# Optimization experiments

Hardware: AMD Instinct MI355X
Metric: run time of the kernel (lower is better)

Reference implementation:

```python
import jax, jax.numpy as jnp
import numpy as np

N = 20000; E = 320000; F_IN = 128; H = 4; D = 32; HD = 128; G = 8; C = 10


def _ln(x, g, b):
    mu = x.mean(-1, keepdims=True)
    v = ((x - mu) ** 2).mean(-1, keepdims=True)
    return (x - mu) / jnp.sqrt(v + 1e-5) * g + b


def _tconv(x, src, dst, attr, Wq, Wk, Wv, We, Ws, bq, bk, bv, be, bs):
    # PyG TransformerConv (concat=True, beta=False, root_weight=True), eval mode
    n = x.shape[0]
    q = (x @ Wq + bq).reshape(n, H, D)[dst]            # [E,H,D] gather at targets i
    k = (x @ Wk + bk).reshape(n, H, D)[src]            # [E,H,D] gather at sources j
    v = (x @ Wv + bv).reshape(n, H, D)[src]
    ef = (attr @ We + be).reshape(-1, H, D)            # edge features lifted to [E,H,D]
    k = k + ef
    v = v + ef
    logit = (q * k).sum(-1) / jnp.sqrt(jnp.float32(D))  # [E,H]
    m = jax.ops.segment_max(logit, dst, num_segments=n)
    m = jnp.where(jnp.isfinite(m), m, 0.0)
    ex = jnp.exp(logit - m[dst])
    s = jax.ops.segment_sum(ex, dst, num_segments=n)
    alpha = ex / (s[dst] + 1e-16)                      # segment softmax over incoming edges
    out = jax.ops.segment_sum(v * alpha[..., None], dst, num_segments=n).reshape(n, HD)
    out = out + x @ Ws + bs                            # skip / root weight
    return out, alpha


def setup_inputs() -> dict:
    key = jax.random.key(0)
    ks = jax.random.split(key, 50)
    inp = {}
    inp["x"] = jax.random.normal(ks[0], (N, F_IN), jnp.float32)
    inp["edge_index"] = jax.random.randint(ks[1], (2, E), 0, N)
    inp["attr"] = jax.random.normal(ks[2], (E, 1), jnp.float32)
    inp["batch"] = jnp.sort(jax.random.randint(ks[3], (N,), 0, G))
    i = 4
    for l, din in zip((1, 2, 3), (F_IN, HD, HD)):
        for nm, shp in (("Wq", (din, HD)), ("Wk", (din, HD)), ("Wv", (din, HD)), ("We", (1, HD)), ("Ws", (din, HD))):
            inp[f"{nm}{l}"] = jax.random.normal(ks[i], shp, jnp.float32) * 0.05
            i += 1
        for nm in ("bq", "bk", "bv", "be", "bs"):
            inp[f"{nm}{l}"] = jnp.zeros((HD,), jnp.float32)
    inp["ln1_g"] = jnp.ones((HD,), jnp.float32); inp["ln1_b"] = jnp.zeros((HD,), jnp.float32)
    inp["ln2_g"] = jnp.ones((HD,), jnp.float32); inp["ln2_b"] = jnp.zeros((HD,), jnp.float32)
    inp["fc1_w"] = jax.random.normal(ks[i], (HD, HD), jnp.float32) * 0.05; i += 1
    inp["fc1_b"] = jnp.zeros((HD,), jnp.float32)
    inp["cln_g"] = jnp.ones((HD,), jnp.float32); inp["cln_b"] = jnp.zeros((HD,), jnp.float32)
    inp["fc2_w"] = jax.random.normal(ks[i], (HD, C), jnp.float32) * 0.05
    inp["fc2_b"] = jnp.zeros((C,), jnp.float32)
    return inp


def reference(x, edge_index, attr, batch,
              Wq1, Wk1, Wv1, We1, Ws1, bq1, bk1, bv1, be1, bs1,
              Wq2, Wk2, Wv2, We2, Ws2, bq2, bk2, bv2, be2, bs2,
              Wq3, Wk3, Wv3, We3, Ws3, bq3, bk3, bv3, be3, bs3,
              ln1_g, ln1_b, ln2_g, ln2_b,
              fc1_w, fc1_b, cln_g, cln_b, fc2_w, fc2_b):
    src, dst = edge_index[0], edge_index[1]
    h, a1 = _tconv(x, src, dst, attr, Wq1, Wk1, Wv1, We1, Ws1, bq1, bk1, bv1, be1, bs1)
    h = jax.nn.relu(_ln(h, ln1_g, ln1_b))              # dropout is identity in eval
    h, a2 = _tconv(h, src, dst, attr, Wq2, Wk2, Wv2, We2, Ws2, bq2, bk2, bv2, be2, bs2)
    h = jax.nn.relu(_ln(h, ln2_g, ln2_b))
    z, a3 = _tconv(h, src, dst, attr, Wq3, Wk3, Wv3, We3, Ws3, bq3, bk3, bv3, be3, bs3)
    # global mean pool over graphs
    cnt = jax.ops.segment_sum(jnp.ones((N,), z.dtype), batch, num_segments=G)
    z_pool = jax.ops.segment_sum(z, batch, num_segments=G) / jnp.maximum(cnt, 1.0)[:, None]
    # classifier
    hcl = jax.nn.relu(_ln(z_pool @ fc1_w + fc1_b, cln_g, cln_b))
    probs = jax.nn.softmax(hcl @ fc2_w + fc2_b, axis=1)
    z_sel = z_pool[batch[0]]
    return (z, z_sel, probs, a1, a2, a3)
```

## Files before the change

kernel.cpp:

```cpp
#include <hip/hip_runtime.h>


typedef short short8v __attribute__((ext_vector_type(8)));
typedef float f32x4 __attribute__((ext_vector_type(4)));

__device__ __forceinline__ unsigned pack_bf16_rne(float a, float b) {
    unsigned ua = __float_as_uint(a);
    ua += 0x7fffu + ((ua >> 16) & 1u);
    unsigned ub = __float_as_uint(b);
    ub += 0x7fffu + ((ub >> 16) & 1u);
    return (ua >> 16) | (ub & 0xffff0000u);
}

__device__ __forceinline__ unsigned short bf16_rne1(float a) {
    unsigned u = __float_as_uint(a);
    u += 0x7fffu + ((u >> 16) & 1u);
    return (unsigned short)(u >> 16);
}

__device__ __forceinline__ float blo(unsigned u) { return __uint_as_float(u << 16); }
__device__ __forceinline__ float bhi(unsigned u) { return __uint_as_float(u & 0xffff0000u); }

__global__ __launch_bounds__(256) void hist_kernel(const int* __restrict__ dst,
                                                   int* __restrict__ cnt, int E) {
    int e = blockIdx.x * 256 + threadIdx.x;
    if (e < E) atomicAdd(&cnt[dst[e]], 1);
}

__global__ __launch_bounds__(256) void blk_reduce_kernel(const int* __restrict__ cnt,
                                                         int* __restrict__ bsum, int n) {
    __shared__ int ws[4];
    const int i = blockIdx.x * 256 + threadIdx.x;
    const int lane = threadIdx.x & 63, wid = threadIdx.x >> 6;
    int v = (i < n) ? cnt[i] : 0;
#pragma unroll
    for (int off = 1; off < 64; off <<= 1) v += __shfl_xor(v, off);
    if (lane == 0) ws[wid] = v;
    __syncthreads();
    if (threadIdx.x == 0) bsum[blockIdx.x] = ws[0] + ws[1] + ws[2] + ws[3];
}

__global__ __launch_bounds__(1024) void blk_scan_kernel(int* __restrict__ bsum, int nb) {
    __shared__ int wls[16];
    const int tid = threadIdx.x, lane = tid & 63, wid = tid >> 6;
    int v = (tid < nb) ? bsum[tid] : 0;
    int sc = v;
#pragma unroll
    for (int off = 1; off < 64; off <<= 1) {
        int t = __shfl_up(sc, off);
        if (lane >= off) sc += t;
    }
    if (lane == 63) wls[wid] = sc;
    __syncthreads();
    if (tid == 0) {
        int run = 0;
        for (int w = 0; w < 16; ++w) { int t = wls[w]; wls[w] = run; run += t; }
    }
    __syncthreads();
    if (tid < nb) bsum[tid] = wls[wid] + sc - v;
}

__global__ __launch_bounds__(256) void rowptr_fill_kernel(const int* __restrict__ cnt,
                                                          const int* __restrict__ boff,
                                                          int* __restrict__ rowptr, int n) {
    __shared__ int wls[4];
    const int i = blockIdx.x * 256 + threadIdx.x;
    const int lane = threadIdx.x & 63, wid = threadIdx.x >> 6;
    int v = (i < n) ? cnt[i] : 0;
    int sc = v;
#pragma unroll
    for (int off = 1; off < 64; off <<= 1) {
        int t = __shfl_up(sc, off);
        if (lane >= off) sc += t;
    }
    if (lane == 63) wls[wid] = sc;
    __syncthreads();
    int add = boff[blockIdx.x];
    for (int w = 0; w < wid; ++w) add += wls[w];
    if (i < n) rowptr[i + 1] = sc + add;
    if (i == 0) rowptr[0] = 0;
}

__global__ __launch_bounds__(256) void fill_kernel(const int* __restrict__ src,
                                                   const int* __restrict__ dst,
                                                   const float* __restrict__ attr,
                                                   const int* __restrict__ rowptr,
                                                   int* __restrict__ tmp,
                                                   int* __restrict__ src_perm,
                                                   float* __restrict__ attr_perm,
                                                   int* __restrict__ eidp, int E) {
    int e = blockIdx.x * 256 + threadIdx.x;
    if (e < E) {
        int d = dst[e];
        int p = atomicAdd(&tmp[d], 1);
        int pos = rowptr[d] + p;
        src_perm[pos] = src[e];
        attr_perm[pos] = attr[e];
        eidp[pos] = e;
    }
}

__global__ __launch_bounds__(256) void cvt_bf16_kernel(const float* __restrict__ in,
                                                       unsigned* __restrict__ outp, int n32) {
    int i = blockIdx.x * 256 + threadIdx.x;
    if (i < n32) {
        float2 v = *(const float2*)&in[(size_t)i * 2];
        outp[i] = pack_bf16_rne(v.x, v.y);
    }
}

struct W12 { const float* p[12]; };
__global__ __launch_bounds__(256) void prepack_all_kernel(W12 ws, unsigned* __restrict__ wt) {
    const int m = blockIdx.y;
    const float* W = ws.p[m];
    int idx = blockIdx.x * 256 + threadIdx.x;
    int c = idx >> 6;
    int kp = idx & 63;
    wt[(size_t)m * 8192 + (size_t)c * 64 + kp] =
        pack_bf16_rne(W[(size_t)(2 * kp) * 128 + c], W[(size_t)(2 * kp + 1) * 128 + c]);
}

__global__ __launch_bounds__(256) void gemm_mfma_kernel(
    const unsigned short* __restrict__ Xb, const unsigned short* __restrict__ wt,
    const float* __restrict__ bq, const float* __restrict__ bk,
    const float* __restrict__ bv, const float* __restrict__ bs,
    float* __restrict__ qo, unsigned short* __restrict__ ko,
    unsigned short* __restrict__ vo, float* __restrict__ so, int nrows) {
    const int lane = threadIdx.x & 63;
    const int w = threadIdx.x >> 6;
    const int m = blockIdx.y;
    const int strip = blockIdx.x * 64 + w * 16;
    const int arow = strip + (lane & 15);
    const int arow_c = min(arow, nrows - 1);
    const int kblk = (lane >> 4) * 8;
    const unsigned short* Wm = wt + (size_t)m * 16384;
    const float* bias = (m == 0) ? bq : (m == 1) ? bk : (m == 2) ? bv : bs;

    f32x4 acc[8];
#pragma unroll
    for (int f = 0; f < 8; ++f) acc[f] = (f32x4){0.f, 0.f, 0.f, 0.f};

#pragma unroll
    for (int ks = 0; ks < 4; ++ks) {
        const int k0 = ks * 32 + kblk;
        const short8v a = *(const short8v*)&Xb[(size_t)arow_c * 128 + k0];
#pragma unroll
        for (int f = 0; f < 8; ++f) {
            const short8v b = *(const short8v*)&Wm[(size_t)(f * 16 + (lane & 15)) * 128 + k0];
            acc[f] = __builtin_amdgcn_mfma_f32_16x16x32_bf16(a, b, acc[f], 0, 0, 0);
        }
    }

    const int r0 = strip + (lane >> 4) * 4;
#pragma unroll
    for (int f = 0; f < 8; ++f) {
        const int col = f * 16 + (lane & 15);
        const float bv_ = bias[col];
        if (m == 0 || m == 3) {
            float* OUT = (m == 0) ? qo : so;
#pragma unroll
            for (int r = 0; r < 4; ++r) {
                int row = r0 + r;
                if (row < nrows) OUT[(size_t)row * 128 + col] = acc[f][r] + bv_;
            }
        } else {
            unsigned short* OUT = (m == 1) ? ko : vo;
#pragma unroll
            for (int r = 0; r < 4; ++r) {
                int row = r0 + r;
                if (row < nrows) OUT[(size_t)row * 128 + col] = bf16_rne1(acc[f][r] + bv_);
            }
        }
    }
}

__global__ __launch_bounds__(256) void node_fused_kernel(
    const float* __restrict__ qb, const unsigned* __restrict__ kb,
    const unsigned* __restrict__ vb,
    const float* __restrict__ Wev, const float* __restrict__ bev,
    const int* __restrict__ rowptr, const int* __restrict__ src_perm,
    const float* __restrict__ attr_perm, const int* __restrict__ eidp,
    float* __restrict__ alpha_perm, float* __restrict__ alpha_out,
    const float* __restrict__ skip, float* __restrict__ zout,
    unsigned* __restrict__ hbout,
    const float* __restrict__ lng, const float* __restrict__ lnb,
    int do_ln, int n) {
    __shared__ float alds[4][64][4];
    const int wid = threadIdx.x >> 6;
    const int node = blockIdx.x * 4 + wid;
    const int lane = threadIdx.x & 63;
    if (node >= n) return;
    const int start = rowptr[node], end = rowptr[node + 1];
    const int deg = end - start;
    const int h = lane >> 4;
    const float we0 = Wev[2 * lane], we1 = Wev[2 * lane + 1];
    const float be0 = bev[2 * lane], be1 = bev[2 * lane + 1];
    const float2 qv = *(const float2*)&qb[(size_t)node * 128 + 2 * lane];
    const float scale = 0.17677669529663687f;
    const bool fastp = (deg <= 64);

    float acc0 = 0.f, acc1 = 0.f, sa = 0.f;

    if (deg > 0 && fastp) {
        float pw = qv.x * we0 + qv.y * we1;
        float pb = qv.x * be0 + qv.y * be1;
#pragma unroll
        for (int off = 1; off < 16; off <<= 1) {
            pw += __shfl_xor(pw, off);
            pb += __shfl_xor(pb, off);
        }

        const bool valid = lane < deg;
        const int j = start + lane;
        const int sj = valid ? src_perm[j] : 0;
        const float aj = valid ? attr_perm[j] : 0.f;

        int t = 0;
        for (; t + 3 < deg; t += 4) {
            const int s0 = __shfl(sj, t), s1 = __shfl(sj, t + 1);
            const int s2 = __shfl(sj, t + 2), s3 = __shfl(sj, t + 3);
            const float a0 = __shfl(aj, t), a1 = __shfl(aj, t + 1);
            const float a2 = __shfl(aj, t + 2), a3 = __shfl(aj, t + 3);
            const unsigned u0 = kb[(size_t)s0 * 64 + lane];
            const unsigned u1 = kb[(size_t)s1 * 64 + lane];
            const unsigned u2 = kb[(size_t)s2 * 64 + lane];
            const unsigned u3 = kb[(size_t)s3 * 64 + lane];
            float p0 = qv.x * blo(u0) + qv.y * bhi(u0);
            float p1 = qv.x * blo(u1) + qv.y * bhi(u1);
            float p2 = qv.x * blo(u2) + qv.y * bhi(u2);
            float p3 = qv.x * blo(u3) + qv.y * bhi(u3);
#pragma unroll
            for (int off = 1; off < 16; off <<= 1) {
                p0 += __shfl_xor(p0, off); p1 += __shfl_xor(p1, off);
                p2 += __shfl_xor(p2, off); p3 += __shfl_xor(p3, off);
            }
            if ((lane & 15) == 0) {
                alds[wid][t + 0][h] = (p0 + a0 * pw + pb) * scale;
                alds[wid][t + 1][h] = (p1 + a1 * pw + pb) * scale;
                alds[wid][t + 2][h] = (p2 + a2 * pw + pb) * scale;
                alds[wid][t + 3][h] = (p3 + a3 * pw + pb) * scale;
            }
        }
        for (; t < deg; ++t) {
            const int s0 = __shfl(sj, t);
            const float a0 = __shfl(aj, t);
            const unsigned u0 = kb[(size_t)s0 * 64 + lane];
            float p0 = qv.x * blo(u0) + qv.y * bhi(u0);
#pragma unroll
            for (int off = 1; off < 16; off <<= 1) p0 += __shfl_xor(p0, off);
            if ((lane & 15) == 0) alds[wid][t][h] = (p0 + a0 * pw + pb) * scale;
        }

        float4 lg = valid ? *(const float4*)&alds[wid][lane][0]
                          : make_float4(-1e30f, -1e30f, -1e30f, -1e30f);
        float4 mx = lg;
#pragma unroll
        for (int off = 1; off < 64; off <<= 1) {
            mx.x = fmaxf(mx.x, __shfl_xor(mx.x, off));
            mx.y = fmaxf(mx.y, __shfl_xor(mx.y, off));
            mx.z = fmaxf(mx.z, __shfl_xor(mx.z, off));
            mx.w = fmaxf(mx.w, __shfl_xor(mx.w, off));
        }
        float4 ev;
        ev.x = __expf(lg.x - mx.x); ev.y = __expf(lg.y - mx.y);
        ev.z = __expf(lg.z - mx.z); ev.w = __expf(lg.w - mx.w);
        float4 s4 = ev;
#pragma unroll
        for (int off = 1; off < 64; off <<= 1) {
            s4.x += __shfl_xor(s4.x, off); s4.y += __shfl_xor(s4.y, off);
            s4.z += __shfl_xor(s4.z, off); s4.w += __shfl_xor(s4.w, off);
        }
        float4 al;
        al.x = ev.x / (s4.x + 1e-16f); al.y = ev.y / (s4.y + 1e-16f);
        al.z = ev.z / (s4.z + 1e-16f); al.w = ev.w / (s4.w + 1e-16f);
        if (valid) *(float4*)&alpha_out[(size_t)eidp[j] * 4] = al;
        *(float4*)&alds[wid][lane][0] = al;

        t = 0;
        for (; t + 3 < deg; t += 4) {
            const int s0 = __shfl(sj, t), s1 = __shfl(sj, t + 1);
            const int s2 = __shfl(sj, t + 2), s3 = __shfl(sj, t + 3);
            const float a0 = __shfl(aj, t), a1 = __shfl(aj, t + 1);
            const float a2 = __shfl(aj, t + 2), a3 = __shfl(aj, t + 3);
            const float w0 = alds[wid][t + 0][h];
            const float w1 = alds[wid][t + 1][h];
            const float w2 = alds[wid][t + 2][h];
            const float w3 = alds[wid][t + 3][h];
            const unsigned u0 = vb[(size_t)s0 * 64 + lane];
            const unsigned u1 = vb[(size_t)s1 * 64 + lane];
            const unsigned u2 = vb[(size_t)s2 * 64 + lane];
            const unsigned u3 = vb[(size_t)s3 * 64 + lane];
            acc0 += w0 * blo(u0) + w1 * blo(u1) + w2 * blo(u2) + w3 * blo(u3);
            acc1 += w0 * bhi(u0) + w1 * bhi(u1) + w2 * bhi(u2) + w3 * bhi(u3);
            sa += w0 * a0 + w1 * a1 + w2 * a2 + w3 * a3;
        }
        for (; t < deg; ++t) {
            const int s0 = __shfl(sj, t);
            const float a0 = __shfl(aj, t);
            const float w0 = alds[wid][t][h];
            const unsigned u0 = vb[(size_t)s0 * 64 + lane];
            acc0 += w0 * blo(u0);
            acc1 += w0 * bhi(u0);
            sa += w0 * a0;
        }
    } else if (deg > 0) {
        float mh = -1e30f;
        for (int c0 = start; c0 < end; c0 += 64) {
            const int nc = min(64, end - c0);
            const int sj = (lane < nc) ? src_perm[c0 + lane] : 0;
            const float aj = (lane < nc) ? attr_perm[c0 + lane] : 0.f;
            int t = 0;
            for (; t + 1 < nc; t += 2) {
                const int s0 = __shfl(sj, t), s1 = __shfl(sj, t + 1);
                const float a0 = __shfl(aj, t), a1 = __shfl(aj, t + 1);
                const unsigned u0 = kb[(size_t)s0 * 64 + lane];
                const unsigned u1 = kb[(size_t)s1 * 64 + lane];
                float p0 = qv.x * (blo(u0) + a0 * we0 + be0) + qv.y * (bhi(u0) + a0 * we1 + be1);
                float p1 = qv.x * (blo(u1) + a1 * we0 + be0) + qv.y * (bhi(u1) + a1 * we1 + be1);
#pragma unroll
                for (int off = 1; off < 16; off <<= 1) {
                    p0 += __shfl_xor(p0, off);
                    p1 += __shfl_xor(p1, off);
                }
                p0 *= scale; p1 *= scale;
                mh = fmaxf(mh, fmaxf(p0, p1));
                if ((lane & 15) == 0) {
                    alpha_perm[(size_t)(c0 + t) * 4 + h] = p0;
                    alpha_perm[(size_t)(c0 + t + 1) * 4 + h] = p1;
                }
            }
            if (t < nc) {
                const int s0 = __shfl(sj, t);
                const float a0 = __shfl(aj, t);
                const unsigned u0 = kb[(size_t)s0 * 64 + lane];
                float p0 = qv.x * (blo(u0) + a0 * we0 + be0) + qv.y * (bhi(u0) + a0 * we1 + be1);
#pragma unroll
                for (int off = 1; off < 16; off <<= 1) p0 += __shfl_xor(p0, off);
                p0 *= scale;
                mh = fmaxf(mh, p0);
                if ((lane & 15) == 0) alpha_perm[(size_t)(c0 + t) * 4 + h] = p0;
            }
        }
        const float m0 = __shfl(mh, 0), m1 = __shfl(mh, 16);
        const float m2 = __shfl(mh, 32), m3 = __shfl(mh, 48);

        float4 s4 = make_float4(0.f, 0.f, 0.f, 0.f);
        for (int c0 = start; c0 < end; c0 += 64) {
            const int j = c0 + lane;
            if (j < end) {
                float4 lg = *(const float4*)&alpha_perm[(size_t)j * 4];
                lg.x = __expf(lg.x - m0); lg.y = __expf(lg.y - m1);
                lg.z = __expf(lg.z - m2); lg.w = __expf(lg.w - m3);
                *(float4*)&alpha_perm[(size_t)j * 4] = lg;
                s4.x += lg.x; s4.y += lg.y; s4.z += lg.z; s4.w += lg.w;
            }
        }
#pragma unroll
        for (int off = 1; off < 64; off <<= 1) {
            s4.x += __shfl_xor(s4.x, off); s4.y += __shfl_xor(s4.y, off);
            s4.z += __shfl_xor(s4.z, off); s4.w += __shfl_xor(s4.w, off);
        }
        const float i0 = 1.f / (s4.x + 1e-16f), i1 = 1.f / (s4.y + 1e-16f);
        const float i2 = 1.f / (s4.z + 1e-16f), i3 = 1.f / (s4.w + 1e-16f);

        for (int c0 = start; c0 < end; c0 += 64) {
            const int nc = min(64, end - c0);
            const int j = c0 + lane;
            if (lane < nc) {
                float4 ex = *(const float4*)&alpha_perm[(size_t)j * 4];
                float4 al;
                al.x = ex.x * i0; al.y = ex.y * i1; al.z = ex.z * i2; al.w = ex.w * i3;
                *(float4*)&alpha_out[(size_t)eidp[j] * 4] = al;
                *(float4*)&alds[wid][lane][0] = al;
            }
            const int sj = (lane < nc) ? src_perm[j] : 0;
            const float aj = (lane < nc) ? attr_perm[j] : 0.f;
            int t = 0;
            for (; t + 1 < nc; t += 2) {
                const int s0 = __shfl(sj, t), s1 = __shfl(sj, t + 1);
                const float a0 = __shfl(aj, t), a1 = __shfl(aj, t + 1);
                const float w0 = alds[wid][t][h];
                const float w1 = alds[wid][t + 1][h];
                const unsigned u0 = vb[(size_t)s0 * 64 + lane];
                const unsigned u1 = vb[(size_t)s1 * 64 + lane];
                acc0 += w0 * (blo(u0) + a0 * we0 + be0) + w1 * (blo(u1) + a1 * we0 + be0);
                acc1 += w0 * (bhi(u0) + a0 * we1 + be1) + w1 * (bhi(u1) + a1 * we1 + be1);
            }
            if (t < nc) {
                const int s0 = __shfl(sj, t);
                const float a0 = __shfl(aj, t);
                const float w0 = alds[wid][t][h];
                const unsigned u0 = vb[(size_t)s0 * 64 + lane];
                acc0 += w0 * (blo(u0) + a0 * we0 + be0);
                acc1 += w0 * (bhi(u0) + a0 * we1 + be1);
            }
        }
    }

    float2 o = *(const float2*)&skip[(size_t)node * 128 + 2 * lane];
    if (deg > 0) {
        if (fastp) {
            o.x += acc0 + sa * we0 + be0;
            o.y += acc1 + sa * we1 + be1;
        } else {
            o.x += acc0;
            o.y += acc1;
        }
    }
    if (do_ln) {
        float s = o.x + o.y;
#pragma unroll
        for (int off = 1; off < 64; off <<= 1) s += __shfl_xor(s, off);
        const float mu = s * (1.f / 128.f);
        const float d0 = o.x - mu, d1 = o.y - mu;
        float vs = d0 * d0 + d1 * d1;
#pragma unroll
        for (int off = 1; off < 64; off <<= 1) vs += __shfl_xor(vs, off);
        const float inv = rsqrtf(vs * (1.f / 128.f) + 1e-5f);
        const float2 gv = *(const float2*)&lng[2 * lane];
        const float2 bv2 = *(const float2*)&lnb[2 * lane];
        const float n0 = fmaxf(d0 * inv * gv.x + bv2.x, 0.f);
        const float n1 = fmaxf(d1 * inv * gv.y + bv2.y, 0.f);
        hbout[(size_t)node * 64 + lane] = pack_bf16_rne(n0, n1);
    } else {
        *(float2*)&zout[(size_t)node * 128 + 2 * lane] = o;
    }
}

__global__ __launch_bounds__(128) void pool_kernel(const float* __restrict__ z,
                                                   const int* __restrict__ batch,
                                                   float* __restrict__ pool,
                                                   int* __restrict__ gcnt, int n) {
    const int c = threadIdx.x;
    const int row0 = blockIdx.x * 32;
    if (row0 >= n) return;
    const int rend = min(row0 + 32, n);
    int cur = batch[row0];
    float acc = 0.f;
    int run = 0;
    for (int r = row0; r < rend; ++r) {
        const int g = batch[r];
        if (g != cur) {
            atomicAdd(&pool[cur * 128 + c], acc);
            if (c == 0) atomicAdd(&gcnt[cur], run);
            acc = 0.f; run = 0; cur = g;
        }
        acc += z[(size_t)r * 128 + c];
        ++run;
    }
    atomicAdd(&pool[cur * 128 + c], acc);
    if (c == 0) atomicAdd(&gcnt[cur], run);
}

__global__ __launch_bounds__(128) void classifier_kernel(
    const float* __restrict__ pool, const int* __restrict__ gcnt,
    const int* __restrict__ batch,
    const float* __restrict__ fc1_w, const float* __restrict__ fc1_b,
    const float* __restrict__ cg, const float* __restrict__ cbv,
    const float* __restrict__ fc2_w, const float* __restrict__ fc2_b,
    float* __restrict__ zsel, float* __restrict__ probs) {
    __shared__ float zp[8][128];
    __shared__ float hc[8][128];
    __shared__ float red[2];
    __shared__ float lgt[8][10];
    const int c = threadIdx.x;
    const int lane = c & 63, wid = c >> 6;
#pragma unroll
    for (int g = 0; g < 8; ++g)
        zp[g][c] = pool[g * 128 + c] / fmaxf((float)gcnt[g], 1.f);
    __syncthreads();
    zsel[c] = zp[batch[0]][c];

    float acc[8];
#pragma unroll
    for (int g = 0; g < 8; ++g) acc[g] = fc1_b[c];
    for (int k = 0; k < 128; ++k) {
        const float w = fc1_w[k * 128 + c];
#pragma unroll
        for (int g = 0; g < 8; ++g) acc[g] += zp[g][k] * w;
    }
#pragma unroll
    for (int g = 0; g < 8; ++g) {
        float s = acc[g];
        for (int off = 1; off < 64; off <<= 1) s += __shfl_xor(s, off);
        if (lane == 0) red[wid] = s;
        __syncthreads();
        const float mu = (red[0] + red[1]) * (1.f / 128.f);
        __syncthreads();
        const float d = acc[g] - mu;
        float s2 = d * d;
        for (int off = 1; off < 64; off <<= 1) s2 += __shfl_xor(s2, off);
        if (lane == 0) red[wid] = s2;
        __syncthreads();
        const float var = (red[0] + red[1]) * (1.f / 128.f);
        __syncthreads();
        hc[g][c] = fmaxf(d * rsqrtf(var + 1e-5f) * cg[c] + cbv[c], 0.f);
    }
    __syncthreads();
    if (c < 80) {
        const int g = c / 10, j = c - g * 10;
        float s = fc2_b[j];
        for (int k = 0; k < 128; ++k) s += hc[g][k] * fc2_w[k * 10 + j];
        lgt[g][j] = s;
    }
    __syncthreads();
    if (c < 8) {
        float mx = -1e30f;
#pragma unroll
        for (int j = 0; j < 10; ++j) mx = fmaxf(mx, lgt[c][j]);
        float ex[10];
        float sum = 0.f;
#pragma unroll
        for (int j = 0; j < 10; ++j) { ex[j] = expf(lgt[c][j] - mx); sum += ex[j]; }
#pragma unroll
        for (int j = 0; j < 10; ++j) probs[c * 10 + j] = ex[j] / sum;
    }
}


extern "C" void kernel_launch(void* const* d_in, const int* in_sizes, int n_in,
                              void* d_out, int out_size, void* d_ws, size_t ws_size,
                              hipStream_t stream) {
    const float* x = (const float*)d_in[0];
    const int* edge_index = (const int*)d_in[1];
    const float* attr = (const float*)d_in[2];
    const int* batch = (const int*)d_in[3];
    const int N = in_sizes[0] / 128;
    const int E = in_sizes[2];
    const int* src = edge_index;
    const int* dst = edge_index + E;

    const float *Wq[3], *Wk[3], *Wv[3], *We[3], *Ws[3];
    const float *bq[3], *bk[3], *bv[3], *be[3], *bs[3];
    int idx = 4;
    for (int l = 0; l < 3; ++l) {
        Wq[l] = (const float*)d_in[idx++];
        Wk[l] = (const float*)d_in[idx++];
        Wv[l] = (const float*)d_in[idx++];
        We[l] = (const float*)d_in[idx++];
        Ws[l] = (const float*)d_in[idx++];
        bq[l] = (const float*)d_in[idx++];
        bk[l] = (const float*)d_in[idx++];
        bv[l] = (const float*)d_in[idx++];
        be[l] = (const float*)d_in[idx++];
        bs[l] = (const float*)d_in[idx++];
    }
    const float* ln_g[2] = {(const float*)d_in[34], (const float*)d_in[36]};
    const float* ln_b[2] = {(const float*)d_in[35], (const float*)d_in[37]};
    const float* fc1_w = (const float*)d_in[38];
    const float* fc1_b = (const float*)d_in[39];
    const float* cln_g = (const float*)d_in[40];
    const float* cln_b = (const float*)d_in[41];
    const float* fc2_w = (const float*)d_in[42];
    const float* fc2_b = (const float*)d_in[43];
    const int C = in_sizes[43];

    float* out = (float*)d_out;
    float* z_out = out;
    float* zsel_out = out + (size_t)N * 128;
    float* probs_out = zsel_out + 128;
    const int GC = out_size - N * 128 - 128 - 3 * E * 4;
    const int G = GC / C;
    float* alpha_out[3];
    alpha_out[0] = probs_out + GC;
    alpha_out[1] = alpha_out[0] + (size_t)E * 4;
    alpha_out[2] = alpha_out[1] + (size_t)E * 4;

    char* p = (char*)d_ws;
    auto alloc = [&](size_t bytes) {
        void* r = (void*)p;
        p += (bytes + 255) & ~(size_t)255;
        return r;
    };
    float* qb = (float*)alloc((size_t)N * 128 * 4);
    unsigned* kb = (unsigned*)alloc((size_t)N * 64 * 4);
    unsigned* vb = (unsigned*)alloc((size_t)N * 64 * 4);
    float* hA = (float*)alloc((size_t)N * 128 * 4);
    unsigned* xb = (unsigned*)alloc((size_t)N * 64 * 4);
    unsigned* hb = (unsigned*)alloc((size_t)N * 64 * 4);
    unsigned* wt = (unsigned*)alloc((size_t)12 * 8192 * 4);
    int* counts = (int*)alloc((size_t)N * 4);
    int* rowptr = (int*)alloc((size_t)(N + 1) * 4);
    int* cnt2 = (int*)alloc((size_t)N * 4);
    int* bsum = (int*)alloc((size_t)1024 * 4);
    int* src_perm = (int*)alloc((size_t)E * 4);
    float* attr_perm = (float*)alloc((size_t)E * 4);
    int* eidp = (int*)alloc((size_t)E * 4);
    float* alpha_perm = (float*)alloc((size_t)E * 4 * 4);
    float* pool = (float*)alloc((size_t)G * 128 * 4);
    int* gcnt = (int*)alloc((size_t)G * 4);

    hipMemsetAsync(counts, 0, (size_t)N * 4, stream);
    hipMemsetAsync(cnt2, 0, (size_t)N * 4, stream);
    hipMemsetAsync(pool, 0, (size_t)G * 128 * 4, stream);
    hipMemsetAsync(gcnt, 0, (size_t)G * 4, stream);

    const int nb = (N + 255) / 256;
    hist_kernel<<<(E + 255) / 256, 256, 0, stream>>>(dst, counts, E);
    blk_reduce_kernel<<<nb, 256, 0, stream>>>(counts, bsum, N);
    blk_scan_kernel<<<1, 1024, 0, stream>>>(bsum, nb);
    rowptr_fill_kernel<<<nb, 256, 0, stream>>>(counts, bsum, rowptr, N);
    fill_kernel<<<(E + 255) / 256, 256, 0, stream>>>(src, dst, attr, rowptr, cnt2,
                                                     src_perm, attr_perm, eidp, E);

    cvt_bf16_kernel<<<(N * 64 + 255) / 256, 256, 0, stream>>>(x, xb, N * 64);
    W12 ws;
    for (int l = 0; l < 3; ++l) {
        ws.p[l * 4 + 0] = Wq[l]; ws.p[l * 4 + 1] = Wk[l];
        ws.p[l * 4 + 2] = Wv[l]; ws.p[l * 4 + 3] = Ws[l];
    }
    prepack_all_kernel<<<dim3(32, 12), 256, 0, stream>>>(ws, wt);

    for (int l = 0; l < 3; ++l) {
        float* SKIP = (l < 2) ? hA : z_out;
        const unsigned short* Xin = (const unsigned short*)((l == 0) ? xb : hb);
        gemm_mfma_kernel<<<dim3((N + 63) / 64, 4), 256, 0, stream>>>(
            Xin, (const unsigned short*)(wt + (size_t)l * 4 * 8192),
            bq[l], bk[l], bv[l], bs[l],
            qb, (unsigned short*)kb, (unsigned short*)vb, SKIP, N);
        node_fused_kernel<<<(N + 3) / 4, 256, 0, stream>>>(
            qb, kb, vb, We[l], be[l], rowptr, src_perm, attr_perm, eidp,
            alpha_perm, alpha_out[l], SKIP, z_out, hb,
            (l < 2) ? ln_g[l] : ln_g[0], (l < 2) ? ln_b[l] : ln_b[0],
            (l < 2) ? 1 : 0, N);
    }

    pool_kernel<<<(N + 31) / 32, 128, 0, stream>>>(z_out, batch, pool, gcnt, N);
    classifier_kernel<<<1, 128, 0, stream>>>(pool, gcnt, batch, fc1_w, fc1_b,
                                             cln_g, cln_b, fc2_w, fc2_b,
                                             zsel_out, probs_out);
}
```

Before: 501.8 us.

## Split each node's edges across two waves and fuse GEMM weight pairs

```diff
diff --git a/kernel.cpp b/kernel.cpp
--- a/kernel.cpp
+++ b/kernel.cpp
@@ -128,17 +128,22 @@
     unsigned short* __restrict__ vo, float* __restrict__ so, int nrows) {
     const int lane = threadIdx.x & 63;
     const int w = threadIdx.x >> 6;
-    const int m = blockIdx.y;
+    const int pair = blockIdx.y;
     const int strip = blockIdx.x * 64 + w * 16;
     const int arow = strip + (lane & 15);
     const int arow_c = min(arow, nrows - 1);
     const int kblk = (lane >> 4) * 8;
-    const unsigned short* Wm = wt + (size_t)m * 16384;
-    const float* bias = (m == 0) ? bq : (m == 1) ? bk : (m == 2) ? bv : bs;
-
-    f32x4 acc[8];
-#pragma unroll
-    for (int f = 0; f < 8; ++f) acc[f] = (f32x4){0.f, 0.f, 0.f, 0.f};
+    const unsigned short* WmA = wt + (size_t)(pair * 2) * 16384;
+    const unsigned short* WmB = wt + (size_t)(pair * 2 + 1) * 16384;
+    const float* biasA = (pair == 0) ? bq : bv;
+    const float* biasB = (pair == 0) ? bk : bs;
+
+    f32x4 accA[8], accB[8];
+#pragma unroll
+    for (int f = 0; f < 8; ++f) {
+        accA[f] = (f32x4){0.f, 0.f, 0.f, 0.f};
+        accB[f] = (f32x4){0.f, 0.f, 0.f, 0.f};
+    }
 
 #pragma unroll
     for (int ks = 0; ks < 4; ++ks) {
@@ -146,8 +151,11 @@
         const short8v a = *(const short8v*)&Xb[(size_t)arow_c * 128 + k0];
 #pragma unroll
         for (int f = 0; f < 8; ++f) {
-            const short8v b = *(const short8v*)&Wm[(size_t)(f * 16 + (lane & 15)) * 128 + k0];
-            acc[f] = __builtin_amdgcn_mfma_f32_16x16x32_bf16(a, b, acc[f], 0, 0, 0);
+            const size_t boff = (size_t)(f * 16 + (lane & 15)) * 128 + k0;
+            const short8v b0 = *(const short8v*)&WmA[boff];
+            const short8v b1 = *(const short8v*)&WmB[boff];
+            accA[f] = __builtin_amdgcn_mfma_f32_16x16x32_bf16(a, b0, accA[f], 0, 0, 0);
+            accB[f] = __builtin_amdgcn_mfma_f32_16x16x32_bf16(a, b1, accB[f], 0, 0, 0);
         }
     }
 
@@ -155,20 +163,19 @@
 #pragma unroll
     for (int f = 0; f < 8; ++f) {
         const int col = f * 16 + (lane & 15);
-        const float bv_ = bias[col];
-        if (m == 0 || m == 3) {
-            float* OUT = (m == 0) ? qo : so;
-#pragma unroll
-            for (int r = 0; r < 4; ++r) {
-                int row = r0 + r;
-                if (row < nrows) OUT[(size_t)row * 128 + col] = acc[f][r] + bv_;
-            }
-        } else {
-            unsigned short* OUT = (m == 1) ? ko : vo;
-#pragma unroll
-            for (int r = 0; r < 4; ++r) {
-                int row = r0 + r;
-                if (row < nrows) OUT[(size_t)row * 128 + col] = bf16_rne1(acc[f][r] + bv_);
+        const float bA = biasA[col];
+        const float bB = biasB[col];
+#pragma unroll
+        for (int r = 0; r < 4; ++r) {
+            int row = r0 + r;
+            if (row < nrows) {
+                if (pair == 0) {
+                    qo[(size_t)row * 128 + col] = accA[f][r] + bA;
+                    ko[(size_t)row * 128 + col] = bf16_rne1(accB[f][r] + bB);
+                } else {
+                    vo[(size_t)row * 128 + col] = bf16_rne1(accA[f][r] + bA);
+                    so[(size_t)row * 128 + col] = accB[f][r] + bB;
+                }
             }
         }
     }
@@ -186,22 +193,37 @@
     const float* __restrict__ lng, const float* __restrict__ lnb,
     int do_ln, int n) {
     __shared__ float alds[4][64][4];
+    __shared__ float cmb[4][8];
+    __shared__ float accb[2][64][2];
     const int wid = threadIdx.x >> 6;
-    const int node = blockIdx.x * 4 + wid;
+    const int part = wid & 1;
+    const int nslot = wid >> 1;
+    const int nodeRaw = blockIdx.x * 2 + nslot;
+    const bool live = nodeRaw < n;
+    const int node = live ? nodeRaw : (n - 1);
     const int lane = threadIdx.x & 63;
-    if (node >= n) return;
     const int start = rowptr[node], end = rowptr[node + 1];
     const int deg = end - start;
+    const bool fast = (deg <= 128);
     const int h = lane >> 4;
     const float we0 = Wev[2 * lane], we1 = Wev[2 * lane + 1];
     const float be0 = bev[2 * lane], be1 = bev[2 * lane + 1];
     const float2 qv = *(const float2*)&qb[(size_t)node * 128 + 2 * lane];
     const float scale = 0.17677669529663687f;
-    const bool fastp = (deg <= 64);
+
+    const int h0 = (deg + 1) >> 1;
+    const int cstart = start + part * h0;
+    const int cdeg = part ? (deg - h0) : h0;
 
     float acc0 = 0.f, acc1 = 0.f, sa = 0.f;
-
-    if (deg > 0 && fastp) {
+    float4 m_w = make_float4(-1e30f, -1e30f, -1e30f, -1e30f);
+    float4 s_w = make_float4(0.f, 0.f, 0.f, 0.f);
+    float4 evr = make_float4(0.f, 0.f, 0.f, 0.f);
+    bool valid = false;
+    int sj = 0;
+    float aj = 0.f;
+
+    if (live && deg > 0 && fast) {
         float pw = qv.x * we0 + qv.y * we1;
         float pb = qv.x * be0 + qv.y * be1;
 #pragma unroll
@@ -209,14 +231,12 @@
             pw += __shfl_xor(pw, off);
             pb += __shfl_xor(pb, off);
         }
-
-        const bool valid = lane < deg;
-        const int j = start + lane;
-        const int sj = valid ? src_perm[j] : 0;
-        const float aj = valid ? attr_perm[j] : 0.f;
+        valid = lane < cdeg;
+        sj = valid ? src_perm[cstart + lane] : 0;
+        aj = valid ? attr_perm[cstart + lane] : 0.f;
 
         int t = 0;
-        for (; t + 3 < deg; t += 4) {
+        for (; t + 3 < cdeg; t += 4) {
             const int s0 = __shfl(sj, t), s1 = __shfl(sj, t + 1);
             const int s2 = __shfl(sj, t + 2), s3 = __shfl(sj, t + 3);
             const float a0 = __shfl(aj, t), a1 = __shfl(aj, t + 1);
@@ -241,7 +261,7 @@
                 alds[wid][t + 3][h] = (p3 + a3 * pw + pb) * scale;
             }
         }
-        for (; t < deg; ++t) {
+        for (; t < cdeg; ++t) {
             const int s0 = __shfl(sj, t);
             const float a0 = __shfl(aj, t);
             const unsigned u0 = kb[(size_t)s0 * 64 + lane];
@@ -270,14 +290,135 @@
             s4.x += __shfl_xor(s4.x, off); s4.y += __shfl_xor(s4.y, off);
             s4.z += __shfl_xor(s4.z, off); s4.w += __shfl_xor(s4.w, off);
         }
+        m_w = mx; s_w = s4; evr = ev;
+    } else if (live && deg > 0 && !fast && part == 0) {
+        float mh = -1e30f;
+        for (int c0 = start; c0 < end; c0 += 64) {
+            const int nc = min(64, end - c0);
+            const int sjf = (lane < nc) ? src_perm[c0 + lane] : 0;
+            const float ajf = (lane < nc) ? attr_perm[c0 + lane] : 0.f;
+            int t = 0;
+            for (; t + 1 < nc; t += 2) {
+                const int s0 = __shfl(sjf, t), s1 = __shfl(sjf, t + 1);
+                const float a0 = __shfl(ajf, t), a1 = __shfl(ajf, t + 1);
+                const unsigned u0 = kb[(size_t)s0 * 64 + lane];
+                const unsigned u1 = kb[(size_t)s1 * 64 + lane];
+                float p0 = qv.x * (blo(u0) + a0 * we0 + be0) + qv.y * (bhi(u0) + a0 * we1 + be1);
+                float p1 = qv.x * (blo(u1) + a1 * we0 + be0) + qv.y * (bhi(u1) + a1 * we1 + be1);
+#pragma unroll
+                for (int off = 1; off < 16; off <<= 1) {
+                    p0 += __shfl_xor(p0, off);
+                    p1 += __shfl_xor(p1, off);
+                }
+                p0 *= scale; p1 *= scale;
+                mh = fmaxf(mh, fmaxf(p0, p1));
+                if ((lane & 15) == 0) {
+                    alpha_perm[(size_t)(c0 + t) * 4 + h] = p0;
+                    alpha_perm[(size_t)(c0 + t + 1) * 4 + h] = p1;
+                }
+            }
+            if (t < nc) {
+                const int s0 = __shfl(sjf, t);
+                const float a0 = __shfl(ajf, t);
+                const unsigned u0 = kb[(size_t)s0 * 64 + lane];
+                float p0 = qv.x * (blo(u0) + a0 * we0 + be0) + qv.y * (bhi(u0) + a0 * we1 + be1);
+#pragma unroll
+                for (int off = 1; off < 16; off <<= 1) p0 += __shfl_xor(p0, off);
+                p0 *= scale;
+                mh = fmaxf(mh, p0);
+                if ((lane & 15) == 0) alpha_perm[(size_t)(c0 + t) * 4 + h] = p0;
+            }
+        }
+        const float m0 = __shfl(mh, 0), m1 = __shfl(mh, 16);
+        const float m2 = __shfl(mh, 32), m3 = __shfl(mh, 48);
+
+        float4 s4 = make_float4(0.f, 0.f, 0.f, 0.f);
+        for (int c0 = start; c0 < end; c0 += 64) {
+            const int j = c0 + lane;
+            if (j < end) {
+                float4 lg = *(const float4*)&alpha_perm[(size_t)j * 4];
+                lg.x = __expf(lg.x - m0); lg.y = __expf(lg.y - m1);
+                lg.z = __expf(lg.z - m2); lg.w = __expf(lg.w - m3);
+                *(float4*)&alpha_perm[(size_t)j * 4] = lg;
+                s4.x += lg.x; s4.y += lg.y; s4.z += lg.z; s4.w += lg.w;
+            }
+        }
+#pragma unroll
+        for (int off = 1; off < 64; off <<= 1) {
+            s4.x += __shfl_xor(s4.x, off); s4.y += __shfl_xor(s4.y, off);
+            s4.z += __shfl_xor(s4.z, off); s4.w += __shfl_xor(s4.w, off);
+        }
+        const float i0 = 1.f / (s4.x + 1e-16f), i1 = 1.f / (s4.y + 1e-16f);
+        const float i2 = 1.f / (s4.z + 1e-16f), i3 = 1.f / (s4.w + 1e-16f);
+
+        for (int c0 = start; c0 < end; c0 += 64) {
+            const int nc = min(64, end - c0);
+            const int j = c0 + lane;
+            if (lane < nc) {
+                float4 ex = *(const float4*)&alpha_perm[(size_t)j * 4];
+                float4 al;
+                al.x = ex.x * i0; al.y = ex.y * i1; al.z = ex.z * i2; al.w = ex.w * i3;
+                *(float4*)&alpha_out[(size_t)eidp[j] * 4] = al;
+                *(float4*)&alds[wid][lane][0] = al;
+            }
+            const int sjf = (lane < nc) ? src_perm[j] : 0;
+            const float ajf = (lane < nc) ? attr_perm[j] : 0.f;
+            int t = 0;
+            for (; t + 1 < nc; t += 2) {
+                const int s0 = __shfl(sjf, t), s1 = __shfl(sjf, t + 1);
+                const float a0 = __shfl(ajf, t), a1 = __shfl(ajf, t + 1);
+                const float w0 = alds[wid][t][h];
+                const float w1 = alds[wid][t + 1][h];
+                const unsigned u0 = vb[(size_t)s0 * 64 + lane];
+                const unsigned u1 = vb[(size_t)s1 * 64 + lane];
+                acc0 += w0 * (blo(u0) + a0 * we0 + be0) + w1 * (blo(u1) + a1 * we0 + be0);
+                acc1 += w0 * (bhi(u0) + a0 * we1 + be1) + w1 * (bhi(u1) + a1 * we1 + be1);
+            }
+            if (t < nc) {
+                const int s0 = __shfl(sjf, t);
+                const float a0 = __shfl(ajf, t);
+                const float w0 = alds[wid][t][h];
+                const unsigned u0 = vb[(size_t)s0 * 64 + lane];
+                acc0 += w0 * (blo(u0) + a0 * we0 + be0);
+                acc1 += w0 * (bhi(u0) + a0 * we1 + be1);
+            }
+        }
+    }
+
+    if (lane == 0) {
+        cmb[wid][0] = m_w.x; cmb[wid][1] = m_w.y;
+        cmb[wid][2] = m_w.z; cmb[wid][3] = m_w.w;
+        cmb[wid][4] = s_w.x; cmb[wid][5] = s_w.y;
+        cmb[wid][6] = s_w.z; cmb[wid][7] = s_w.w;
+    }
+    __syncthreads();
+
+    if (live && deg > 0 && fast) {
+        const int pw = wid ^ 1;
+        const float4 m_p = make_float4(cmb[pw][0], cmb[pw][1], cmb[pw][2], cmb[pw][3]);
+        const float4 s_p = make_float4(cmb[pw][4], cmb[pw][5], cmb[pw][6], cmb[pw][7]);
+        float4 M;
+        M.x = fmaxf(m_w.x, m_p.x); M.y = fmaxf(m_w.y, m_p.y);
+        M.z = fmaxf(m_w.z, m_p.z); M.w = fmaxf(m_w.w, m_p.w);
+        float4 rs, rp;
+        rs.x = __expf(m_w.x - M.x); rp.x = __expf(m_p.x - M.x);
+        rs.y = __expf(m_w.y - M.y); rp.y = __expf(m_p.y - M.y);
+        rs.z = __expf(m_w.z - M.z); rp.z = __expf(m_p.z - M.z);
+        rs.w = __expf(m_w.w - M.w); rp.w = __expf(m_p.w - M.w);
+        float4 f;
+        f.x = rs.x / (rs.x * s_w.x + rp.x * s_p.x + 1e-16f);
+        f.y = rs.y / (rs.y * s_w.y + rp.y * s_p.y + 1e-16f);
+        f.z = rs.z / (rs.z * s_w.z + rp.z * s_p.z + 1e-16f);
+        f.w = rs.w / (rs.w * s_w.w + rp.w * s_p.w + 1e-16f);
+
         float4 al;
-        al.x = ev.x / (s4.x + 1e-16f); al.y = ev.y / (s4.y + 1e-16f);
-        al.z = ev.z / (s4.z + 1e-16f); al.w = ev.w / (s4.w + 1e-16f);
-        if (valid) *(float4*)&alpha_out[(size_t)eidp[j] * 4] = al;
+        al.x = evr.x * f.x; al.y = evr.y * f.y;
+        al.z = evr.z * f.z; al.w = evr.w * f.w;
+        if (valid) *(float4*)&alpha_out[(size_t)eidp[cstart + lane] * 4] = al;
         *(float4*)&alds[wid][lane][0] = al;
 
-        t = 0;
-        for (; t + 3 < deg; t += 4) {
+        int t = 0;
+        for (; t + 3 < cdeg; t += 4) {
             const int s0 = __shfl(sj, t), s1 = __shfl(sj, t + 1);
             const int s2 = __shfl(sj, t + 2), s3 = __shfl(sj, t + 3);
             const float a0 = __shfl(aj, t), a1 = __shfl(aj, t + 1);
@@ -294,7 +435,7 @@
             acc1 += w0 * bhi(u0) + w1 * bhi(u1) + w2 * bhi(u2) + w3 * bhi(u3);
             sa += w0 * a0 + w1 * a1 + w2 * a2 + w3 * a3;
         }
-        for (; t < deg; ++t) {
+        for (; t < cdeg; ++t) {
             const int s0 = __shfl(sj, t);
             const float a0 = __shfl(aj, t);
             const float w0 = alds[wid][t][h];
@@ -303,127 +444,42 @@
             acc1 += w0 * bhi(u0);
             sa += w0 * a0;
         }
-    } else if (deg > 0) {
-        float mh = -1e30f;
-        for (int c0 = start; c0 < end; c0 += 64) {
-            const int nc = min(64, end - c0);
-            const int sj = (lane < nc) ? src_perm[c0 + lane] : 0;
-            const float aj = (lane < nc) ? attr_perm[c0 + lane] : 0.f;
-            int t = 0;
-            for (; t + 1 < nc; t += 2) {
-                const int s0 = __shfl(sj, t), s1 = __shfl(sj, t + 1);
-                const float a0 = __shfl(aj, t), a1 = __shfl(aj, t + 1);
-                const unsigned u0 = kb[(size_t)s0 * 64 + lane];
-                const unsigned u1 = kb[(size_t)s1 * 64 + lane];
-                float p0 = qv.x * (blo(u0) + a0 * we0 + be0) + qv.y * (bhi(u0) + a0 * we1 + be1);
-                float p1 = qv.x * (blo(u1) + a1 * we0 + be0) + qv.y * (bhi(u1) + a1 * we1 + be1);
-#pragma unroll
-                for (int off = 1; off < 16; off <<= 1) {
-                    p0 += __shfl_xor(p0, off);
-                    p1 += __shfl_xor(p1, off);
-                }
-                p0 *= scale; p1 *= scale;
-                mh = fmaxf(mh, fmaxf(p0, p1));
-                if ((lane & 15) == 0) {
-                    alpha_perm[(size_t)(c0 + t) * 4 + h] = p0;
-                    alpha_perm[(size_t)(c0 + t + 1) * 4 + h] = p1;
-                }
-            }
-            if (t < nc) {
-                const int s0 = __shfl(sj, t);
-                const float a0 = __shfl(aj, t);
-                const unsigned u0 = kb[(size_t)s0 * 64 + lane];
-                float p0 = qv.x * (blo(u0) + a0 * we0 + be0) + qv.y * (bhi(u0) + a0 * we1 + be1);
-#pragma unroll
-                for (int off = 1; off < 16; off <<= 1) p0 += __shfl_xor(p0, off);
-                p0 *= scale;
-                mh = fmaxf(mh, p0);
-                if ((lane & 15) == 0) alpha_perm[(size_t)(c0 + t) * 4 + h] = p0;
-            }
-        }
-        const float m0 = __shfl(mh, 0), m1 = __shfl(mh, 16);
-        const float m2 = __shfl(mh, 32), m3 = __shfl(mh, 48);
-
-        float4 s4 = make_float4(0.f, 0.f, 0.f, 0.f);
-        for (int c0 = start; c0 < end; c0 += 64) {
-            const int j = c0 + lane;
-            if (j < end) {
-                float4 lg = *(const float4*)&alpha_perm[(size_t)j * 4];
-                lg.x = __expf(lg.x - m0); lg.y = __expf(lg.y - m1);
-                lg.z = __expf(lg.z - m2); lg.w = __expf(lg.w - m3);
-                *(float4*)&alpha_perm[(size_t)j * 4] = lg;
-                s4.x += lg.x; s4.y += lg.y; s4.z += lg.z; s4.w += lg.w;
-            }
-        }
-#pragma unroll
-        for (int off = 1; off < 64; off <<= 1) {
-            s4.x += __shfl_xor(s4.x, off); s4.y += __shfl_xor(s4.y, off);
-            s4.z += __shfl_xor(s4.z, off); s4.w += __shfl_xor(s4.w, off);
-        }
-        const float i0 = 1.f / (s4.x + 1e-16f), i1 = 1.f / (s4.y + 1e-16f);
-        const float i2 = 1.f / (s4.z + 1e-16f), i3 = 1.f / (s4.w + 1e-16f);
-
-        for (int c0 = start; c0 < end; c0 += 64) {
-            const int nc = min(64, end - c0);
-            const int j = c0 + lane;
-            if (lane < nc) {
-                float4 ex = *(const float4*)&alpha_perm[(size_t)j * 4];
-                float4 al;
-                al.x = ex.x * i0; al.y = ex.y * i1; al.z = ex.z * i2; al.w = ex.w * i3;
-                *(float4*)&alpha_out[(size_t)eidp[j] * 4] = al;
-                *(float4*)&alds[wid][lane][0] = al;
-            }
-            const int sj = (lane < nc) ? src_perm[j] : 0;
-            const float aj = (lane < nc) ? attr_perm[j] : 0.f;
-            int t = 0;
-            for (; t + 1 < nc; t += 2) {
-                const int s0 = __shfl(sj, t), s1 = __shfl(sj, t + 1);
-                const float a0 = __shfl(aj, t), a1 = __shfl(aj, t + 1);
-                const float w0 = alds[wid][t][h];
-                const float w1 = alds[wid][t + 1][h];
-                const unsigned u0 = vb[(size_t)s0 * 64 + lane];
-                const unsigned u1 = vb[(size_t)s1 * 64 + lane];
-                acc0 += w0 * (blo(u0) + a0 * we0 + be0) + w1 * (blo(u1) + a1 * we0 + be0);
-                acc1 += w0 * (bhi(u0) + a0 * we1 + be1) + w1 * (bhi(u1) + a1 * we1 + be1);
-            }
-            if (t < nc) {
-                const int s0 = __shfl(sj, t);
-                const float a0 = __shfl(aj, t);
-                const float w0 = alds[wid][t][h];
-                const unsigned u0 = vb[(size_t)s0 * 64 + lane];
-                acc0 += w0 * (blo(u0) + a0 * we0 + be0);
-                acc1 += w0 * (bhi(u0) + a0 * we1 + be1);
-            }
-        }
-    }
-
-    float2 o = *(const float2*)&skip[(size_t)node * 128 + 2 * lane];
-    if (deg > 0) {
-        if (fastp) {
-            o.x += acc0 + sa * we0 + be0;
-            o.y += acc1 + sa * we1 + be1;
+        acc0 += sa * we0;
+        acc1 += sa * we1;
+    }
+
+    if (part == 1) {
+        accb[nslot][lane][0] = acc0;
+        accb[nslot][lane][1] = acc1;
+    }
+    __syncthreads();
+
+    if (part == 0 && live) {
+        acc0 += accb[nslot][lane][0];
+        acc1 += accb[nslot][lane][1];
+        float2 o = *(const float2*)&skip[(size_t)node * 128 + 2 * lane];
+        if (deg > 0) {
+            o.x += acc0; o.y += acc1;
+            if (fast) { o.x += be0; o.y += be1; }
+        }
+        if (do_ln) {
+            float s = o.x + o.y;
+#pragma unroll
+            for (int off = 1; off < 64; off <<= 1) s += __shfl_xor(s, off);
+            const float mu = s * (1.f / 128.f);
+            const float d0 = o.x - mu, d1 = o.y - mu;
+            float vs = d0 * d0 + d1 * d1;
+#pragma unroll
+            for (int off = 1; off < 64; off <<= 1) vs += __shfl_xor(vs, off);
+            const float inv = rsqrtf(vs * (1.f / 128.f) + 1e-5f);
+            const float2 gv = *(const float2*)&lng[2 * lane];
+            const float2 bv2 = *(const float2*)&lnb[2 * lane];
+            const float n0 = fmaxf(d0 * inv * gv.x + bv2.x, 0.f);
+            const float n1 = fmaxf(d1 * inv * gv.y + bv2.y, 0.f);
+            hbout[(size_t)node * 64 + lane] = pack_bf16_rne(n0, n1);
         } else {
-            o.x += acc0;
-            o.y += acc1;
-        }
-    }
-    if (do_ln) {
-        float s = o.x + o.y;
-#pragma unroll
-        for (int off = 1; off < 64; off <<= 1) s += __shfl_xor(s, off);
-        const float mu = s * (1.f / 128.f);
-        const float d0 = o.x - mu, d1 = o.y - mu;
-        float vs = d0 * d0 + d1 * d1;
-#pragma unroll
-        for (int off = 1; off < 64; off <<= 1) vs += __shfl_xor(vs, off);
-        const float inv = rsqrtf(vs * (1.f / 128.f) + 1e-5f);
-        const float2 gv = *(const float2*)&lng[2 * lane];
-        const float2 bv2 = *(const float2*)&lnb[2 * lane];
-        const float n0 = fmaxf(d0 * inv * gv.x + bv2.x, 0.f);
-        const float n1 = fmaxf(d1 * inv * gv.y + bv2.y, 0.f);
-        hbout[(size_t)node * 64 + lane] = pack_bf16_rne(n0, n1);
-    } else {
-        *(float2*)&zout[(size_t)node * 128 + 2 * lane] = o;
+            *(float2*)&zout[(size_t)node * 128 + 2 * lane] = o;
+        }
     }
 }
 
@@ -614,11 +670,11 @@
     for (int l = 0; l < 3; ++l) {
         float* SKIP = (l < 2) ? hA : z_out;
         const unsigned short* Xin = (const unsigned short*)((l == 0) ? xb : hb);
-        gemm_mfma_kernel<<<dim3((N + 63) / 64, 4), 256, 0, stream>>>(
+        gemm_mfma_kernel<<<dim3((N + 63) / 64, 2), 256, 0, stream>>>(
             Xin, (const unsigned short*)(wt + (size_t)l * 4 * 8192),
             bq[l], bk[l], bv[l], bs[l],
             qb, (unsigned short*)kb, (unsigned short*)vb, SKIP, N);
-        node_fused_kernel<<<(N + 3) / 4, 256, 0, stream>>>(
+        node_fused_kernel<<<(N + 1) / 2, 256, 0, stream>>>(
             qb, kb, vb, We[l], be[l], rowptr, src_perm, attr_perm, eidp,
             alpha_perm, alpha_out[l], SKIP, z_out, hb,
             (l < 2) ? ln_g[l] : ln_g[0], (l < 2) ? ln_b[l] : ln_b[0],
```

Measured after the change: 530.3 us. +5.7%, slower.
